# Optimization experiments

Hardware: AMD Instinct MI355X
Metric: run time of the kernel (lower is better)

## Reference

```python
import jax, jax.numpy as jnp
import numpy as np

IN_DIM = 100
OUT_DIM = 200
N_ETYPES = 4
N_STEPS = 8
CONCAT = IN_DIM + OUT_DIM  # 300
EPS = 1e-5


def setup_inputs() -> dict:
    key = jax.random.key(0)
    ks = jax.random.split(key, 24)
    N, E = 100000, 1600000
    rn = lambda k, shape, s=0.05: jax.random.normal(k, shape, dtype=jnp.float32) * s
    return {
        "features": rn(ks[0], (N, IN_DIM), 1.0),
        "edge_index": jax.random.randint(ks[1], (2, E), 0, N, dtype=jnp.int32),
        "edge_types": jax.random.randint(ks[2], (E,), 0, N_ETYPES, dtype=jnp.int32),
        "ggnn_W": rn(ks[3], (N_ETYPES, OUT_DIM, OUT_DIM)),
        "ggnn_b": rn(ks[4], (N_ETYPES, OUT_DIM)),
        "gru_Wih": rn(ks[5], (3 * OUT_DIM, OUT_DIM)),
        "gru_Whh": rn(ks[6], (3 * OUT_DIM, OUT_DIM)),
        "gru_bih": rn(ks[7], (3 * OUT_DIM,)),
        "gru_bhh": rn(ks[8], (3 * OUT_DIM,)),
        "conv1_w": rn(ks[9], (OUT_DIM, OUT_DIM, 3)),
        "conv1_b": rn(ks[10], (OUT_DIM,)),
        "conv2_w": rn(ks[11], (OUT_DIM, OUT_DIM, 1)),
        "conv2_b": rn(ks[12], (OUT_DIM,)),
        "convc1_w": rn(ks[13], (CONCAT, CONCAT, 3)),
        "convc1_b": rn(ks[14], (CONCAT,)),
        "convc2_w": rn(ks[15], (CONCAT, CONCAT, 1)),
        "convc2_b": rn(ks[16], (CONCAT,)),
        "bn_y_g": jnp.ones((OUT_DIM,), jnp.float32),
        "bn_y_b": jnp.zeros((OUT_DIM,), jnp.float32),
        "bn_c_g": jnp.ones((CONCAT,), jnp.float32),
        "bn_c_b": jnp.zeros((CONCAT,), jnp.float32),
        "mlp_y_w": rn(ks[17], (2, OUT_DIM)),
        "mlp_y_b": rn(ks[18], (2,)),
        "mlp_z_w": rn(ks[19], (2, CONCAT)),
        "mlp_z_b": rn(ks[20], (2,)),
    }


def _ggnn(features, src, dst, etypes, W, b, Wih, Whh, bih, bhh):
    """DGL-style GatedGraphConv: per-etype linear, sum-aggregate, GRU update."""
    N = features.shape[0]
    h0 = jnp.concatenate(
        [features, jnp.zeros((N, OUT_DIM - IN_DIM), features.dtype)], axis=-1)

    def step(h, _):
        # transform every node by every etype weight: [n_etypes, N, OUT_DIM]
        t = jnp.einsum('koh,nh->kno', W, h) + b[:, None, :]
        msg = t[etypes, src]                         # [E, OUT_DIM] gather
        a = jax.ops.segment_sum(msg, dst, num_segments=N)  # scatter-add
        # torch GRUCell
        gi = a @ Wih.T + bih
        gh = h @ Whh.T + bhh
        ir, iz, inn = jnp.split(gi, 3, axis=-1)
        hr, hz, hn = jnp.split(gh, 3, axis=-1)
        r = jax.nn.sigmoid(ir + hr)
        z = jax.nn.sigmoid(iz + hz)
        n = jnp.tanh(inn + r * hn)
        return (1.0 - z) * n + z * h, None

    h, _ = jax.lax.scan(step, h0, None, length=N_STEPS)
    return h


def _bn(x, g, b):  # x: [1, C, L], training-mode BatchNorm1d (biased var)
    m = x.mean(axis=(0, 2), keepdims=True)
    v = x.var(axis=(0, 2), keepdims=True)
    return (x - m) * jax.lax.rsqrt(v + EPS) * g[None, :, None] + b[None, :, None]


def _conv1d(x, w, b):  # x: [N, C, L], w: [O, I, k]
    y = jax.lax.conv_general_dilated(
        x, w, window_strides=(1,), padding='VALID',
        dimension_numbers=('NCH', 'OIH', 'NCH'))
    return y + b[None, :, None]


def _maxpool1d(x, k, s):
    return jax.lax.reduce_window(x, -jnp.inf, jax.lax.max,
                                 (1, 1, k), (1, 1, s), 'VALID')


def reference(features, edge_index, edge_types, ggnn_W, ggnn_b,
              gru_Wih, gru_Whh, gru_bih, gru_bhh,
              conv1_w, conv1_b, conv2_w, conv2_b,
              convc1_w, convc1_b, convc2_w, convc2_b,
              bn_y_g, bn_y_b, bn_c_g, bn_c_b,
              mlp_y_w, mlp_y_b, mlp_z_w, mlp_z_b):
    src, dst = edge_index[0], edge_index[1]
    out = _ggnn(features, src, dst, edge_types, ggnn_W, ggnn_b,
                gru_Wih, gru_Whh, gru_bih, gru_bhh)   # [N, 200]
    x_i = features[None]            # [1, N, 100]
    h_i = out[None]                 # [1, N, 200]
    c_i = jnp.concatenate([h_i, x_i], axis=-1)  # [1, N, 300]

    y = _maxpool1d(jax.nn.relu(_bn(_conv1d(jnp.swapaxes(h_i, 1, 2), conv1_w, conv1_b), bn_y_g, bn_y_b)), 3, 2)
    Y2 = jnp.swapaxes(_maxpool1d(jax.nn.relu(_bn(_conv1d(y, conv2_w, conv2_b), bn_y_g, bn_y_b)), 2, 2), 1, 2)

    z = _maxpool1d(jax.nn.relu(_bn(_conv1d(jnp.swapaxes(c_i, 1, 2), convc1_w, convc1_b), bn_c_g, bn_c_b)), 3, 2)
    Z2 = jnp.swapaxes(_maxpool1d(jax.nn.relu(_bn(_conv1d(z, convc2_w, convc2_b), bn_c_g, bn_c_b)), 2, 2), 1, 2)

    before_avg = (Y2 @ mlp_y_w.T + mlp_y_b) * (Z2 @ mlp_z_w.T + mlp_z_b)  # [1, L, 2]
    return jax.nn.sigmoid(before_avg.mean(axis=1))  # [1, 2]
```

## Files before the change

kernel.cpp:

```cpp
#include <hip/hip_runtime.h>
#include <cstddef>
#include <cstdint>


typedef unsigned short u16;
typedef unsigned char u8;
typedef __attribute__((ext_vector_type(8))) short bf16x8;
typedef __attribute__((ext_vector_type(4))) float f32x4;
typedef __attribute__((ext_vector_type(2))) float f32x2;

static __device__ __forceinline__ float bf2f(u16 u) {
  union { unsigned int i; float f; } v; v.i = ((unsigned int)u) << 16; return v.f;
}
static __device__ __forceinline__ u16 f2bf(float f) {
  union { float f; unsigned int i; } v; v.f = f;
  unsigned int r = v.i + 0x7FFFu + ((v.i >> 16) & 1u);
  return (u16)(r >> 16);
}
static __device__ __forceinline__ float sigm(float x) { return 1.f / (1.f + __expf(-x)); }
static __device__ __forceinline__ u8 f2fp8(float x) {
  return (u8)(__builtin_amdgcn_cvt_pk_fp8_f32(x, 0.f, 0, false) & 0xff);
}

static __device__ __forceinline__ void gload16(const void* gp, void* lp) {
  __builtin_amdgcn_global_load_lds(
      (const __attribute__((address_space(1))) void*)gp,
      (__attribute__((address_space(3))) void*)lp, 16, 0, 0);
}

__global__ void fail_k(float* out, float code) { out[0] = code; out[1] = code; }

__global__ void init_hb_k(const float* __restrict__ feat, u16* __restrict__ hb, int N) {
  int total = N * 224;
  for (int i = blockIdx.x * blockDim.x + threadIdx.x; i < total; i += blockDim.x * gridDim.x) {
    int n = i / 224, c = i - n * 224;
    hb[i] = (c < 100) ? f2bf(feat[(size_t)n * 100 + c]) : (u16)0;
  }
}

__global__ void init_hq_k(const float* __restrict__ feat, u8* __restrict__ ahq, int N) {
  int total = N * 224;
  for (int i = blockIdx.x * blockDim.x + threadIdx.x; i < total; i += blockDim.x * gridDim.x) {
    int n = i / 224, c = i - n * 224;
    ahq[(size_t)n * 448 + 224 + c] = (c < 100) ? f2fp8(feat[(size_t)n * 100 + c]) : (u8)0;
  }
}

__global__ void count_deg_k(const int* __restrict__ dst, const int* __restrict__ et,
                            int* __restrict__ deg_et, int N, int E) {
  for (int e = blockIdx.x * blockDim.x + threadIdx.x; e < E; e += blockDim.x * gridDim.x)
    atomicAdd(&deg_et[et[e] * N + dst[e]], 1);
}

__global__ __launch_bounds__(1024) void bsum_k(const int* __restrict__ cnt,
                                               int* __restrict__ bsum, int L) {
  __shared__ int buf[1024];
  int i = blockIdx.x * 1024 + threadIdx.x;
  buf[threadIdx.x] = (i < L) ? cnt[i] : 0;
  __syncthreads();
  for (int o = 512; o > 0; o >>= 1) {
    if (threadIdx.x < o) buf[threadIdx.x] += buf[threadIdx.x + o];
    __syncthreads();
  }
  if (threadIdx.x == 0) bsum[blockIdx.x] = buf[0];
}

__global__ __launch_bounds__(1024) void scanb_k(int* __restrict__ bsum, int nb) {
  __shared__ int buf[1024];
  int v = (threadIdx.x < nb) ? bsum[threadIdx.x] : 0;
  buf[threadIdx.x] = v;
  __syncthreads();
  for (int o = 1; o < 1024; o <<= 1) {
    int t = (threadIdx.x >= o) ? buf[threadIdx.x - o] : 0;
    __syncthreads();
    buf[threadIdx.x] += t;
    __syncthreads();
  }
  if (threadIdx.x < nb) bsum[threadIdx.x] = buf[threadIdx.x] - v;
}

__global__ __launch_bounds__(1024) void scan_fin_k(const int* __restrict__ cnt,
                                                   const int* __restrict__ bsum,
                                                   int* __restrict__ off, int L) {
  __shared__ int buf[1024];
  int i = blockIdx.x * 1024 + threadIdx.x;
  int v = (i < L) ? cnt[i] : 0;
  buf[threadIdx.x] = v;
  __syncthreads();
  for (int o = 1; o < 1024; o <<= 1) {
    int t = (threadIdx.x >= o) ? buf[threadIdx.x - o] : 0;
    __syncthreads();
    buf[threadIdx.x] += t;
    __syncthreads();
  }
  if (i < L) off[i] = buf[threadIdx.x] - v + bsum[blockIdx.x];
}

__global__ void copy_int_k(const int* __restrict__ a, int* __restrict__ b, int n) {
  for (int i = blockIdx.x * blockDim.x + threadIdx.x; i < n; i += blockDim.x * gridDim.x) b[i] = a[i];
}

__global__ void fill_src_k(const int* __restrict__ src, const int* __restrict__ dst,
                           const int* __restrict__ et, int* __restrict__ cursor,
                           int* __restrict__ esrc, int N, int E) {
  for (int e = blockIdx.x * blockDim.x + threadIdx.x; e < E; e += blockDim.x * gridDim.x) {
    int p = atomicAdd(&cursor[et[e] * N + dst[e]], 1);
    esrc[p] = src[e];
  }
}


__global__ void pack_wcat8_k(const float* __restrict__ W, const float* __restrict__ gb,
                             u8* __restrict__ dst) {
  int total = 200 * 832;
  for (int i = blockIdx.x * blockDim.x + threadIdx.x; i < total; i += blockDim.x * gridDim.x) {
    int o = i / 832, kp = i - o * 832;
    float v = 0.f;
    if (kp < 800) { int k = kp / 200, kk = kp - k * 200; v = W[((size_t)k * 200 + o) * 200 + kk]; }
    else if (kp < 804) v = gb[(kp - 800) * 200 + o];
    dst[i] = f2fp8(v);
  }
}

__global__ void pack_wall8_k(const float* __restrict__ Wih, const float* __restrict__ Whh,
                             u8* __restrict__ dst) {
  int total = 800 * 448;
  for (int i = blockIdx.x * blockDim.x + threadIdx.x; i < total; i += blockDim.x * gridDim.x) {
    int jp = i / 448, kp = i - jp * 448;
    int o = jp >> 2, g = jp & 3;
    float v = 0.f;
    if (g == 0) {
      if (kp < 200) v = Wih[(size_t)o * 200 + kp];
      else if (kp >= 224 && kp < 424) v = Whh[(size_t)o * 200 + (kp - 224)];
    } else if (g == 1) {
      if (kp < 200) v = Wih[(size_t)(200 + o) * 200 + kp];
      else if (kp >= 224 && kp < 424) v = Whh[(size_t)(200 + o) * 200 + (kp - 224)];
    } else if (g == 2) {
      if (kp < 200) v = Wih[(size_t)(400 + o) * 200 + kp];
    } else {
      if (kp >= 224 && kp < 424) v = Whh[(size_t)(400 + o) * 200 + (kp - 224)];
    }
    dst[i] = f2fp8(v);
  }
}

__global__ void ball_i_k(const float* __restrict__ bih, const float* __restrict__ bhh,
                         float* __restrict__ ball) {
  int j = blockIdx.x * blockDim.x + threadIdx.x;
  if (j < 800) {
    int o = j >> 2, g = j & 3;
    float v;
    if (g == 0) v = bih[o] + bhh[o];
    else if (g == 1) v = bih[200 + o] + bhh[200 + o];
    else if (g == 2) v = bih[400 + o];
    else v = bhh[400 + o];
    ball[j] = v;
  }
}

__global__ void pack_lin_b(const float* __restrict__ src, u16* __restrict__ dst,
                           int Nn, int K, int Kp) {
  int total = Nn * Kp;
  for (int i = blockIdx.x * blockDim.x + threadIdx.x; i < total; i += blockDim.x * gridDim.x) {
    int o = i / Kp, kp = i - o * Kp;
    dst[i] = (kp < K) ? f2bf(src[(size_t)o * K + kp]) : (u16)0;
  }
}

__global__ void pack_w1c_k(const float* __restrict__ src, u16* __restrict__ dst) {
  int total = 200 * 1056;
  for (int i = blockIdx.x * blockDim.x + threadIdx.x; i < total; i += blockDim.x * gridDim.x) {
    int o = i / 1056, r = i - o * 1056;
    int t = r / 352, kp = r - t * 352;
    dst[i] = (kp < 200) ? f2bf(src[((size_t)o * 200 + kp) * 3 + t]) : (u16)0;
  }
}

__global__ void pack_wc1_b(const float* __restrict__ src, u16* __restrict__ dst) {
  int total = 300 * 1056;
  for (int i = blockIdx.x * blockDim.x + threadIdx.x; i < total; i += blockDim.x * gridDim.x) {
    int o = i / 1056, r = i - o * 1056;
    int t = r / 352, kp = r - t * 352;
    int ci = (kp < 224) ? (kp < 200 ? kp : -1) : ((kp - 224) < 100 ? 200 + (kp - 224) : -1);
    dst[i] = (ci >= 0) ? f2bf(src[((size_t)o * 300 + ci) * 3 + t]) : (u16)0;
  }
}

__global__ void agg8_k(const int* __restrict__ off_et, const int* __restrict__ deg_et,
                       const int* __restrict__ esrc, const u8* __restrict__ ahq,
                       u8* __restrict__ scat8, int N) {
  int gtid = blockIdx.x * blockDim.x + threadIdx.x;
  int wid = gtid >> 6, lane = threadIdx.x & 63;
  int nw = (blockDim.x * gridDim.x) >> 6;
  int sub = lane >> 4, l = lane & 15;
  int total = N * 4;
  for (int u = wid; u < total; u += nw) {
    int n = u >> 2, k = u & 3;
    u8* srow = scat8 + (size_t)n * 832;
    int rs = off_et[(size_t)k * N + n], d = deg_et[(size_t)k * N + n];
    f32x2 a2[8];
#pragma unroll
    for (int j = 0; j < 8; ++j) a2[j] = (f32x2)0.f;
    if (l < 13) {
      for (int i = sub; i < d; i += 4) {
        const u8* hr = ahq + (size_t)esrc[rs + i] * 448 + 224 + l * 16;
        uint4 v = *reinterpret_cast<const uint4*>(hr);
        a2[0] += __builtin_amdgcn_cvt_pk_f32_fp8(v.x, 0);
        a2[1] += __builtin_amdgcn_cvt_pk_f32_fp8(v.x, 1);
        a2[2] += __builtin_amdgcn_cvt_pk_f32_fp8(v.y, 0);
        a2[3] += __builtin_amdgcn_cvt_pk_f32_fp8(v.y, 1);
        a2[4] += __builtin_amdgcn_cvt_pk_f32_fp8(v.z, 0);
        a2[5] += __builtin_amdgcn_cvt_pk_f32_fp8(v.z, 1);
        a2[6] += __builtin_amdgcn_cvt_pk_f32_fp8(v.w, 0);
        a2[7] += __builtin_amdgcn_cvt_pk_f32_fp8(v.w, 1);
      }
    }
#pragma unroll
    for (int j = 0; j < 8; ++j) {
      a2[j][0] += __shfl_xor(a2[j][0], 16);
      a2[j][1] += __shfl_xor(a2[j][1], 16);
      a2[j][0] += __shfl_xor(a2[j][0], 32);
      a2[j][1] += __shfl_xor(a2[j][1], 32);
    }
    if (sub == 0 && l < 13) {
      int d0, d1, d2, d3;
      d0 = __builtin_amdgcn_cvt_pk_fp8_f32(a2[0][0], a2[0][1], 0, false);
      d0 = __builtin_amdgcn_cvt_pk_fp8_f32(a2[1][0], a2[1][1], d0, true);
      d1 = __builtin_amdgcn_cvt_pk_fp8_f32(a2[2][0], a2[2][1], 0, false);
      d1 = __builtin_amdgcn_cvt_pk_fp8_f32(a2[3][0], a2[3][1], d1, true);
      *reinterpret_cast<uint2*>(srow + k * 200 + l * 16) = make_uint2(d0, d1);
      if (l < 12) {
        d2 = __builtin_amdgcn_cvt_pk_fp8_f32(a2[4][0], a2[4][1], 0, false);
        d2 = __builtin_amdgcn_cvt_pk_fp8_f32(a2[5][0], a2[5][1], d2, true);
        d3 = __builtin_amdgcn_cvt_pk_fp8_f32(a2[6][0], a2[6][1], 0, false);
        d3 = __builtin_amdgcn_cvt_pk_fp8_f32(a2[7][0], a2[7][1], d3, true);
        *reinterpret_cast<uint2*>(srow + k * 200 + l * 16 + 8) = make_uint2(d2, d3);
      }
    }
    if (k == 0 && lane == 13) {
      float g0 = (float)deg_et[(size_t)0 * N + n];
      float g1 = (float)deg_et[(size_t)1 * N + n];
      float g2 = (float)deg_et[(size_t)2 * N + n];
      float g3 = (float)deg_et[(size_t)3 * N + n];
      int rr = __builtin_amdgcn_cvt_pk_fp8_f32(g0, g1, 0, false);
      rr = __builtin_amdgcn_cvt_pk_fp8_f32(g2, g3, rr, true);
      *reinterpret_cast<unsigned*>(srow + 800) = (unsigned)rr;
    }
    if (k == 3 && lane >= 32 && lane < 39)
      *reinterpret_cast<unsigned*>(srow + 804 + (lane - 32) * 4) = 0;
  }
}

__global__ __launch_bounds__(512, 4) void gemm_a8(
    const u8* __restrict__ A, int lda,
    const u8* __restrict__ B, int ldb,
    u8* __restrict__ Cq, int ldcb, int npad,
    int M, int Nn, int K, int gyr) {
  const int gx = gridDim.x;
  int lin = blockIdx.y * gx + blockIdx.x;
  int k8 = lin & 7, j = lin >> 3;
  int band = gridDim.y >> 3;
  int yy = j / gx, xx = j - yy * gx;
  int by = k8 * band + yy;
  if (by >= gyr) return;
  const int m0 = by * 256, n0 = xx * 128;

  __shared__ __align__(16) u8 As[3 * 8192];
  __shared__ __align__(16) u8 Bs[3 * 4096];
  const int tid = threadIdx.x;
  const int lane = tid & 63;
  const int w = tid >> 6;
  const int wr = w >> 1, wc = w & 1;
  const int fr = lane & 15;
  const int g = lane >> 4;

  const int rowA = tid >> 1;
  const int cA = (tid & 1) ^ (rowA & 1);
  int gaA = m0 + rowA; if (gaA >= M) gaA = M - 1;
  const u8* pa = A + (size_t)gaA * lda + cA * 16;
  u8* lA = &As[(size_t)(w * 64) * 16];
  const int sB = w * 32 + (lane & 31);
  const int rowB = sB >> 1;
  const int cB = (sB & 1) ^ (rowB & 1);
  int gbB = n0 + rowB; if (gbB >= Nn) gbB = Nn - 1;
  const u8* pb = B + (size_t)gbB * ldb + cB * 16;
  u8* lB = &Bs[(size_t)(w * 32) * 16];
  const bool doB = (lane < 32);

  const int rdoff = (((g >> 1) ^ (fr & 1)) << 4) + ((g & 1) << 3);

  f32x4 acc[4][4] = {};
  const int nt = K >> 5;
  const int ABUF = 8192, BBUF = 4096;

  gload16(pa, lA);
  if (doB) gload16(pb, lB);
  pa += 32; pb += 32;
  if (nt > 1) {
    gload16(pa, lA + ABUF);
    if (doB) gload16(pb, lB + BBUF);
    pa += 32; pb += 32;
  }

  for (int t = 0; t < nt; ++t) {
    if (t + 1 < nt) asm volatile("s_waitcnt vmcnt(2)" ::: "memory");
    else            asm volatile("s_waitcnt vmcnt(0)" ::: "memory");
    __builtin_amdgcn_s_barrier();
    if (t + 2 < nt) {
      int bi = (t + 2) % 3;
      gload16(pa, lA + bi * ABUF);
      if (doB) gload16(pb, lB + bi * BBUF);
      pa += 32; pb += 32;
    }
    int ca = (t % 3) * ABUF, cbb = (t % 3) * BBUF;
    long af[4], bfv[4];
#pragma unroll
    for (int i = 0; i < 4; ++i) {
      int row = wr * 64 + i * 16 + fr;
      af[i] = *reinterpret_cast<const long*>(&As[ca + row * 32 + rdoff]);
    }
#pragma unroll
    for (int jj = 0; jj < 4; ++jj) {
      int row = wc * 64 + jj * 16 + fr;
      bfv[jj] = *reinterpret_cast<const long*>(&Bs[cbb + row * 32 + rdoff]);
    }
    __builtin_amdgcn_s_setprio(1);
#pragma unroll
    for (int i = 0; i < 4; ++i)
#pragma unroll
      for (int jj = 0; jj < 4; ++jj)
        acc[i][jj] = __builtin_amdgcn_mfma_f32_16x16x32_fp8_fp8(af[i], bfv[jj], acc[i][jj], 0, 0, 0);
    __builtin_amdgcn_s_setprio(0);
  }

  const int er = (lane >> 4) * 4;
  const int ec = lane & 15;
#pragma unroll
  for (int i = 0; i < 4; ++i) {
#pragma unroll
    for (int jj = 0; jj < 4; ++jj) {
      int n = n0 + wc * 64 + jj * 16 + ec;
#pragma unroll
      for (int r = 0; r < 4; ++r) {
        int m = m0 + wr * 64 + i * 16 + er + r;
        if (m >= M) continue;
        if (n < Nn) Cq[(size_t)m * ldcb + n] = f2fp8(acc[i][jj][r]);
        else if (n < npad) Cq[(size_t)m * ldcb + n] = (u8)0;
      }
    }
  }
}

__global__ __launch_bounds__(512, 4) void gemm_gru8(
    const u8* __restrict__ A, int lda,
    const u8* __restrict__ B, int ldb,
    int M, int K, const float* __restrict__ bias,
    u16* __restrict__ hb, u8* __restrict__ hq, int gyr) {
  const int gx = gridDim.x;
  int lin = blockIdx.y * gx + blockIdx.x;
  int k8 = lin & 7, j = lin >> 3;
  int band = gridDim.y >> 3;
  int yy = j / gx, xx = j - yy * gx;
  int by = k8 * band + yy;
  if (by >= gyr) return;
  const int m0 = by * 256, n0 = xx * 128;
  const int Nn = 800;

  __shared__ __align__(16) u8 SM8[65536];
  u8* As = SM8;
  u8* Bs = SM8 + 24576;
  const int tid = threadIdx.x;
  const int lane = tid & 63;
  const int w = tid >> 6;
  const int wr = w >> 1, wc = w & 1;
  const int fr = lane & 15;
  const int g = lane >> 4;

  const int rowA = tid >> 1;
  const int cA = (tid & 1) ^ (rowA & 1);
  int gaA = m0 + rowA; if (gaA >= M) gaA = M - 1;
  const u8* pa = A + (size_t)gaA * lda + cA * 16;
  u8* lA = &As[(size_t)(w * 64) * 16];
  const int sB = w * 32 + (lane & 31);
  const int rowB = sB >> 1;
  const int cB = (sB & 1) ^ (rowB & 1);
  int gbB = n0 + rowB; if (gbB >= Nn) gbB = Nn - 1;
  const u8* pb = B + (size_t)gbB * ldb + cB * 16;
  u8* lB = &Bs[(size_t)(w * 32) * 16];
  const bool doB = (lane < 32);

  const int rdoff = (((g >> 1) ^ (fr & 1)) << 4) + ((g & 1) << 3);

  f32x4 acc[4][4] = {};
  const int nt = K >> 5;
  const int ABUF = 8192, BBUF = 4096;

  gload16(pa, lA);
  if (doB) gload16(pb, lB);
  pa += 32; pb += 32;
  if (nt > 1) {
    gload16(pa, lA + ABUF);
    if (doB) gload16(pb, lB + BBUF);
    pa += 32; pb += 32;
  }

  for (int t = 0; t < nt; ++t) {
    if (t + 1 < nt) asm volatile("s_waitcnt vmcnt(2)" ::: "memory");
    else            asm volatile("s_waitcnt vmcnt(0)" ::: "memory");
    __builtin_amdgcn_s_barrier();
    if (t + 2 < nt) {
      int bi = (t + 2) % 3;
      gload16(pa, lA + bi * ABUF);
      if (doB) gload16(pb, lB + bi * BBUF);
      pa += 32; pb += 32;
    }
    int ca = (t % 3) * ABUF, cbb = (t % 3) * BBUF;
    long af[4], bfv[4];
#pragma unroll
    for (int i = 0; i < 4; ++i) {
      int row = wr * 64 + i * 16 + fr;
      af[i] = *reinterpret_cast<const long*>(&As[ca + row * 32 + rdoff]);
    }
#pragma unroll
    for (int jj = 0; jj < 4; ++jj) {
      int row = wc * 64 + jj * 16 + fr;
      bfv[jj] = *reinterpret_cast<const long*>(&Bs[cbb + row * 32 + rdoff]);
    }
    __builtin_amdgcn_s_setprio(1);
#pragma unroll
    for (int i = 0; i < 4; ++i)
#pragma unroll
      for (int jj = 0; jj < 4; ++jj)
        acc[i][jj] = __builtin_amdgcn_mfma_f32_16x16x32_fp8_fp8(af[i], bfv[jj], acc[i][jj], 0, 0, 0);
    __builtin_amdgcn_s_setprio(0);
  }

  const int er = (lane >> 4) * 4;
  const int ec = lane & 15;
  __syncthreads();
  float* ep = (float*)(SM8) + (size_t)w * 2048;

  for (int hh = 0; hh < 2; ++hh) {
#pragma unroll
    for (int jj2 = 0; jj2 < 2; ++jj2) {
      int jj = hh * 2 + jj2;
      int n = n0 + wc * 64 + jj * 16 + ec;
      float bv = (n < 800) ? bias[n] : 0.f;
#pragma unroll
      for (int i = 0; i < 4; ++i)
#pragma unroll
        for (int r = 0; r < 4; ++r) {
          int row_loc = i * 16 + er + r;
          ep[row_loc * 32 + jj2 * 16 + ec] = acc[i][jj][r] + bv;
        }
    }
    __syncthreads();
#pragma unroll
    for (int p = 0; p < 8; ++p) {
      int idx = p * 64 + lane;
      int row = idx >> 3, og = idx & 7;
      int n_base = n0 + wc * 64 + hh * 32 + og * 4;
      int m = m0 + wr * 64 + row;
      if (n_base < 800 && m < M) {
        f32x4 gv = *reinterpret_cast<f32x4*>(&ep[row * 32 + og * 4]);
        float rg = sigm(gv[0]);
        float zg = sigm(gv[1]);
        float x = gv[2] + rg * gv[3];
        float e2 = __expf(2.f * x);
        float nn = (e2 - 1.f) / (e2 + 1.f);
        int o = n_base >> 2;
        float hold = bf2f(hb[(size_t)m * 224 + o]);
        float hv = (1.f - zg) * nn + zg * hold;
        hb[(size_t)m * 224 + o] = f2bf(hv);
        hq[(size_t)m * 224 + o] = f2fp8(hv);
      }
    }
    __syncthreads();
  }
}

__global__ void hcopy8_k(const u8* __restrict__ hq, u8* __restrict__ ahq, int N) {
  int total = N * 50;
  for (int i = blockIdx.x * blockDim.x + threadIdx.x; i < total; i += blockDim.x * gridDim.x) {
    int n = i / 50, o4 = (i - n * 50) * 4;
    *reinterpret_cast<unsigned*>(ahq + (size_t)n * 448 + 224 + o4) =
        *reinterpret_cast<const unsigned*>(hq + (size_t)n * 224 + o4);
  }
}

__global__ __launch_bounds__(512, 4) void gemm_mfma(
    const u16* __restrict__ A, int lda,
    const u16* __restrict__ B, int ldb,
    u16* __restrict__ Cb, int ldcb, int npad,
    int M, int Nn, int K, const float* __restrict__ bias, int gyr) {
  const int gx = gridDim.x;
  int lin = blockIdx.y * gx + blockIdx.x;
  int k8 = lin & 7, j = lin >> 3;
  int band = gridDim.y >> 3;
  int yy = j / gx, xx = j - yy * gx;
  int by = k8 * band + yy;
  if (by >= gyr) return;
  const int m0 = by * 256, n0 = xx * 128;

  __shared__ __align__(16) u16 As[3 * 8192];
  __shared__ __align__(16) u16 Bs[3 * 4096];
  const int tid = threadIdx.x;
  const int lane = tid & 63;
  const int w = tid >> 6;
  const int wr = w >> 1, wc = w & 1;
  const int fr = lane & 15;
  const int g = lane >> 4;

  const int sA0 = w * 64 + lane, sA1 = sA0 + 512, sB = sA0;
  int rA0 = sA0 >> 2, cA0 = (sA0 & 3) ^ ((rA0 >> 1) & 3);
  int rA1 = sA1 >> 2, cA1 = (sA1 & 3) ^ ((rA1 >> 1) & 3);
  int rB  = sB  >> 2, cB  = (sB & 3) ^ ((rB >> 1) & 3);
  int ga0 = m0 + rA0; if (ga0 >= M) ga0 = M - 1;
  int ga1 = m0 + rA1; if (ga1 >= M) ga1 = M - 1;
  int gb  = n0 + rB;  if (gb >= Nn) gb = Nn - 1;
  const u16* pa0 = A + (size_t)ga0 * lda + cA0 * 8;
  const u16* pa1 = A + (size_t)ga1 * lda + cA1 * 8;
  const u16* pb  = B + (size_t)gb  * ldb + cB * 8;
  u16* lA0 = &As[(w * 64) * 8];
  u16* lA1 = &As[(512 + w * 64) * 8];
  u16* lB  = &Bs[(w * 64) * 8];

  const int gxr = g ^ ((fr >> 1) & 3);

  f32x4 acc[4][4] = {};
  const int nt = K >> 5;
  const int ABUF = 8192, BBUF = 4096;

  gload16(pa0, lA0); gload16(pa1, lA1); gload16(pb, lB);
  pa0 += 32; pa1 += 32; pb += 32;
  if (nt > 1) {
    gload16(pa0, lA0 + ABUF); gload16(pa1, lA1 + ABUF); gload16(pb, lB + BBUF);
    pa0 += 32; pa1 += 32; pb += 32;
  }

  for (int t = 0; t < nt; ++t) {
    if (t + 1 < nt) asm volatile("s_waitcnt vmcnt(3)" ::: "memory");
    else            asm volatile("s_waitcnt vmcnt(0)" ::: "memory");
    __builtin_amdgcn_s_barrier();
    if (t + 2 < nt) {
      int bi = (t + 2) % 3;
      gload16(pa0, lA0 + bi * ABUF); gload16(pa1, lA1 + bi * ABUF); gload16(pb, lB + bi * BBUF);
      pa0 += 32; pa1 += 32; pb += 32;
    }
    int ca = (t % 3) * ABUF, cbb = (t % 3) * BBUF;
    bf16x8 af[4], bfv[4];
#pragma unroll
    for (int i = 0; i < 4; ++i) {
      int row = wr * 64 + i * 16 + fr;
      af[i] = *reinterpret_cast<const bf16x8*>(&As[ca + (row * 4 + gxr) * 8]);
    }
#pragma unroll
    for (int jj = 0; jj < 4; ++jj) {
      int row = wc * 64 + jj * 16 + fr;
      bfv[jj] = *reinterpret_cast<const bf16x8*>(&Bs[cbb + (row * 4 + gxr) * 8]);
    }
    __builtin_amdgcn_s_setprio(1);
#pragma unroll
    for (int i = 0; i < 4; ++i)
#pragma unroll
      for (int jj = 0; jj < 4; ++jj)
        acc[i][jj] = __builtin_amdgcn_mfma_f32_16x16x32_bf16(af[i], bfv[jj], acc[i][jj], 0, 0, 0);
    __builtin_amdgcn_s_setprio(0);
  }

  const int er = (lane >> 4) * 4;
  const int ec = lane & 15;
#pragma unroll
  for (int i = 0; i < 4; ++i) {
#pragma unroll
    for (int jj = 0; jj < 4; ++jj) {
      int n = n0 + wc * 64 + jj * 16 + ec;
#pragma unroll
      for (int r = 0; r < 4; ++r) {
        int m = m0 + wr * 64 + i * 16 + er + r;
        if (m >= M) continue;
        if (n < Nn) {
          float v = acc[i][jj][r];
          if (bias) v += bias[n];
          Cb[(size_t)m * ldcb + n] = f2bf(v);
        } else if (n < npad) {
          Cb[(size_t)m * ldcb + n] = (u16)0;
        }
      }
    }
  }
}

__global__ void cmat_k(const u16* __restrict__ hb, const float* __restrict__ feat,
                       u16* __restrict__ c, int N) {
  int total = N * 352;
  for (int i = blockIdx.x * blockDim.x + threadIdx.x; i < total; i += blockDim.x * gridDim.x) {
    int n = i / 352, j = i - n * 352;
    u16 v;
    if (j < 224) v = hb[(size_t)n * 224 + j];
    else { int f = j - 224; v = (f < 100) ? f2bf(feat[(size_t)n * 100 + f]) : (u16)0; }
    c[i] = v;
  }
}

__global__ __launch_bounds__(1024) void bn_stats2_k(const u16* __restrict__ X, int L, int C,
                                                    float* __restrict__ stats) {
  const int Q = 1024 / C;
  const int T = Q * C;
  const int tid = threadIdx.x;
  float s = 0.f, q = 0.f;
  int c = 0;
  if (tid < T) {
    int qi = tid / C; c = tid - qi * C;
    for (size_t r = (size_t)blockIdx.x * Q + qi; r < (size_t)L; r += (size_t)gridDim.x * Q) {
      float v = bf2f(X[r * C + c]);
      s += v; q += v * v;
    }
  }
  __shared__ float sb[304], qb[304];
  for (int cc = tid; cc < C; cc += 1024) { sb[cc] = 0.f; qb[cc] = 0.f; }
  __syncthreads();
  if (tid < T) { atomicAdd(&sb[c], s); atomicAdd(&qb[c], q); }
  __syncthreads();
  for (int cc = tid; cc < C; cc += 1024) {
    atomicAdd(&stats[cc], sb[cc]);
    atomicAdd(&stats[C + cc], qb[cc]);
  }
}

__global__ void bn_fin_k(const float* __restrict__ stats, const float* __restrict__ g,
                         const float* __restrict__ b, int C, float Linv,
                         float* __restrict__ scsh) {
  int c = blockIdx.x * blockDim.x + threadIdx.x;
  if (c < C) {
    float mean = stats[c] * Linv;
    float var = stats[C + c] * Linv - mean * mean;
    float sc = g[c] * rsqrtf(var + 1e-5f);
    scsh[c] = sc;
    scsh[C + c] = b[c] - mean * sc;
  }
}

__global__ void pool_bf_k(const u16* __restrict__ X, int C, const float* __restrict__ scsh,
                          int kw, int stride, u16* __restrict__ Y, int Cpad, int Lout) {
  int total = Lout * Cpad;
  for (int i = blockIdx.x * blockDim.x + threadIdx.x; i < total; i += blockDim.x * gridDim.x) {
    int lp = i / Cpad, c = i - lp * Cpad;
    if (c >= C) { Y[i] = (u16)0; continue; }
    float sc = scsh[c], sh = scsh[C + c];
    int l0 = lp * stride;
    float m = 0.f;
    for (int wq = 0; wq < kw; ++wq)
      m = fmaxf(m, fmaf(bf2f(X[(size_t)(l0 + wq) * C + c]), sc, sh));
    Y[i] = f2bf(m);
  }
}

__global__ void pool_f32_k(const u16* __restrict__ X, int C, const float* __restrict__ scsh,
                           int kw, int stride, float* __restrict__ Y, int Lout) {
  int total = Lout * C;
  for (int i = blockIdx.x * blockDim.x + threadIdx.x; i < total; i += blockDim.x * gridDim.x) {
    int lp = i / C, c = i - lp * C;
    float sc = scsh[c], sh = scsh[C + c];
    int l0 = lp * stride;
    float m = 0.f;
    for (int wq = 0; wq < kw; ++wq)
      m = fmaxf(m, fmaf(bf2f(X[(size_t)(l0 + wq) * C + c]), sc, sh));
    Y[i] = m;
  }
}

__global__ __launch_bounds__(256) void final_dot_k(
    const float* __restrict__ Y2, const float* __restrict__ Z2,
    const float* __restrict__ wy, const float* __restrict__ by,
    const float* __restrict__ wz, const float* __restrict__ bz,
    float* __restrict__ acc, int L) {
  float s0 = 0.f, s1 = 0.f;
  for (int lp = blockIdx.x * blockDim.x + threadIdx.x; lp < L; lp += blockDim.x * gridDim.x) {
    const float* y = Y2 + (size_t)lp * 200;
    const float* z = Z2 + (size_t)lp * 300;
    float d0 = 0.f, d1 = 0.f;
    for (int k = 0; k < 200; ++k) { float v = y[k]; d0 += v * wy[k]; d1 += v * wy[200 + k]; }
    float e0 = 0.f, e1 = 0.f;
    for (int k = 0; k < 300; ++k) { float v = z[k]; e0 += v * wz[k]; e1 += v * wz[300 + k]; }
    s0 += (d0 + by[0]) * (e0 + bz[0]);
    s1 += (d1 + by[1]) * (e1 + bz[1]);
  }
  __shared__ float r0[256], r1[256];
  r0[threadIdx.x] = s0; r1[threadIdx.x] = s1;
  __syncthreads();
  for (int off = 128; off > 0; off >>= 1) {
    if (threadIdx.x < off) { r0[threadIdx.x] += r0[threadIdx.x + off]; r1[threadIdx.x] += r1[threadIdx.x + off]; }
    __syncthreads();
  }
  if (threadIdx.x == 0) { atomicAdd(&acc[0], r0[0]); atomicAdd(&acc[1], r1[0]); }
}

__global__ void final_out_k(const float* __restrict__ acc, float invL, float* __restrict__ out) {
  int j = threadIdx.x;
  if (j < 2) out[j] = 1.f / (1.f + expf(-acc[j] * invL));
}


static inline void gemmL(hipStream_t st, const u16* A, int lda, const u16* B, int ldb,
                         u16* Cb, int ldcb, int npad, int M, int Nn, int K, const float* bias) {
  int ncols = (npad > Nn) ? npad : Nn;
  int gx = (ncols + 127) / 128;
  int gy = (M + 255) / 256;
  int gyp = ((gy + 7) / 8) * 8;
  dim3 g(gx, gyp);
  gemm_mfma<<<g, 512, 0, st>>>(A, lda, B, ldb, Cb, ldcb, npad, M, Nn, K, bias, gy);
}

extern "C" void kernel_launch(void* const* d_in, const int* in_sizes, int n_in,
                              void* d_out, int out_size, void* d_ws, size_t ws_size,
                              hipStream_t stream) {
  (void)n_in; (void)out_size;
  const float* feat    = (const float*)d_in[0];
  const int*   eix     = (const int*)d_in[1];
  const int*   etyp    = (const int*)d_in[2];
  const float* ggnnW   = (const float*)d_in[3];
  const float* ggnnB   = (const float*)d_in[4];
  const float* Wih     = (const float*)d_in[5];
  const float* Whh     = (const float*)d_in[6];
  const float* bih     = (const float*)d_in[7];
  const float* bhh     = (const float*)d_in[8];
  const float* conv1w  = (const float*)d_in[9];
  const float* conv2w  = (const float*)d_in[11];
  const float* convc1w = (const float*)d_in[13];
  const float* convc2w = (const float*)d_in[15];
  const float* bnyg    = (const float*)d_in[17];
  const float* bnyb    = (const float*)d_in[18];
  const float* bncg    = (const float*)d_in[19];
  const float* bncb    = (const float*)d_in[20];
  const float* mlpyw   = (const float*)d_in[21];
  const float* mlpyb   = (const float*)d_in[22];
  const float* mlpzw   = (const float*)d_in[23];
  const float* mlpzb   = (const float*)d_in[24];

  const int N = in_sizes[0] / 100;
  const int E = in_sizes[2];
  const int* src = eix;
  const int* dst = eix + E;

  char* base = (char*)d_ws;
  const size_t AHQ_B = (size_t)N * 448;
  const size_t HB_B  = (size_t)N * 224 * 2;
  const int CH = (N + 1) / 2;
  const size_t SCR_B = (size_t)CH * 1664;

  u8*  ahq = (u8*)base;
  u16* hb  = (u16*)(base + AHQ_B);
  char* R1 = base + AHQ_B + HB_B;
  char* WREG = R1 + SCR_B;

  u8*  Wcat8 = (u8*)WREG;
  u8*  Wall8 = Wcat8 + 166400;
  u16* w1c   = (u16*)(Wall8 + 358400);
  u16* c2b   = w1c + 211200;
  u16* wc1   = c2b + 44800;
  u16* wc2   = wc1 + 316800;
  float* ball  = (float*)(wc2 + 96000);
  float* stats = ball + 832;
  float* scsh  = stats + 600;
  float* acc2  = scsh + 600;
  int* deg_et = (int*)(acc2 + 8);
  int* off_et = deg_et + 4 * (size_t)N;
  int* cursor = off_et + 4 * (size_t)N;
  int* esrc   = cursor + 4 * (size_t)N;
  int* bsum   = esrc + E;
  const int L4 = 4 * N;
  const int NB = (L4 + 1023) / 1024;
  size_t need = (size_t)((char*)(bsum + NB) - base);

  if (ws_size < need) {
    fail_k<<<1, 64, 0, stream>>>((float*)d_out, -(float)(ws_size >> 20));
    return;
  }

  hipMemsetAsync(deg_et, 0, sizeof(int) * 4 * (size_t)N, stream);
  init_hb_k<<<2048, 256, 0, stream>>>(feat, hb, N);
  init_hq_k<<<2048, 256, 0, stream>>>(feat, ahq, N);
  count_deg_k<<<2048, 256, 0, stream>>>(dst, etyp, deg_et, N, E);
  bsum_k<<<NB, 1024, 0, stream>>>(deg_et, bsum, L4);
  scanb_k<<<1, 1024, 0, stream>>>(bsum, NB);
  scan_fin_k<<<NB, 1024, 0, stream>>>(deg_et, bsum, off_et, L4);
  copy_int_k<<<512, 256, 0, stream>>>(off_et, cursor, L4);
  fill_src_k<<<2048, 256, 0, stream>>>(src, dst, etyp, cursor, esrc, N, E);
  pack_wcat8_k<<<651, 256, 0, stream>>>(ggnnW, ggnnB, Wcat8);
  pack_wall8_k<<<1400, 256, 0, stream>>>(Wih, Whh, Wall8);
  ball_i_k<<<4, 256, 0, stream>>>(bih, bhh, ball);
  pack_w1c_k<<<825, 256, 0, stream>>>(conv1w, w1c);
  pack_lin_b<<<175, 256, 0, stream>>>(conv2w, c2b, 200, 200, 224);
  pack_wc1_b<<<1238, 256, 0, stream>>>(convc1w, wc1);
  pack_lin_b<<<375, 256, 0, stream>>>(convc2w, wc2, 300, 300, 320);

  u8* scat8   = (u8*)R1;
  u8* hq_next = (u8*)R1;

  const int gy = (N + 255) / 256;
  const int gyp = ((gy + 7) / 8) * 8;

  for (int step = 0; step < 8; ++step) {
    agg8_k<<<4096, 256, 0, stream>>>(off_et, deg_et, esrc, ahq, scat8, N);
    gemm_a8<<<dim3(2, gyp), 512, 0, stream>>>(scat8, 832, Wcat8, 832,
                                              ahq, 448, 224, N, 200, 832, gy);
    gemm_gru8<<<dim3(7, gyp), 512, 0, stream>>>(ahq, 448, Wall8, 448, N, 448, ball,
                                                hb, hq_next, gy);
    hcopy8_k<<<2048, 256, 0, stream>>>(hq_next, ahq, N);
  }

  const int L1 = N - 2;
  const int L2 = (L1 - 3) / 2 + 1;
  const int L3 = (L2 - 2) / 2 + 1;

  u16* cmat = (u16*)R1;
  u16* out1 = (u16*)base;
  size_t y1_off = (((size_t)L1 * 400) + 255) & ~(size_t)255;
  u16* y1 = (u16*)(base + y1_off);
  size_t o2_off = y1_off + ((((size_t)L2 * 448) + 255) & ~(size_t)255);
  u16* out2 = (u16*)(base + o2_off);
  float* Y2f = (float*)base;
  size_t oc1_off = (((size_t)L3 * 800) + 255) & ~(size_t)255;
  u16* outc1 = (u16*)(base + oc1_off);
  u16* z1 = (u16*)R1;
  size_t oc2_off = (((size_t)L2 * 640) + 255) & ~(size_t)255;
  u16* outc2 = (u16*)(R1 + oc2_off);
  float* Z2f = (float*)(base + oc1_off);

  cmat_k<<<4096, 256, 0, stream>>>(hb, feat, cmat, N);

  gemmL(stream, cmat, 352, w1c, 1056, out1, 200, 200, L1, 200, 1056, nullptr);
  hipMemsetAsync(stats, 0, sizeof(float) * 400, stream);
  bn_stats2_k<<<512, 1024, 0, stream>>>(out1, L1, 200, stats);
  bn_fin_k<<<2, 256, 0, stream>>>(stats, bnyg, bnyb, 200, 1.f / (float)L1, scsh);
  pool_bf_k<<<2048, 256, 0, stream>>>(out1, 200, scsh, 3, 2, y1, 224, L2);

  gemmL(stream, y1, 224, c2b, 224, out2, 200, 200, L2, 200, 224, nullptr);
  hipMemsetAsync(stats, 0, sizeof(float) * 400, stream);
  bn_stats2_k<<<512, 1024, 0, stream>>>(out2, L2, 200, stats);
  bn_fin_k<<<2, 256, 0, stream>>>(stats, bnyg, bnyb, 200, 1.f / (float)L2, scsh);
  pool_f32_k<<<2048, 256, 0, stream>>>(out2, 200, scsh, 2, 2, Y2f, L3);

  gemmL(stream, cmat, 352, wc1, 1056, outc1, 300, 300, L1, 300, 1056, nullptr);
  hipMemsetAsync(stats, 0, sizeof(float) * 600, stream);
  bn_stats2_k<<<512, 1024, 0, stream>>>(outc1, L1, 300, stats);
  bn_fin_k<<<2, 256, 0, stream>>>(stats, bncg, bncb, 300, 1.f / (float)L1, scsh);
  pool_bf_k<<<2048, 256, 0, stream>>>(outc1, 300, scsh, 3, 2, z1, 320, L2);

  gemmL(stream, z1, 320, wc2, 320, outc2, 300, 300, L2, 300, 320, nullptr);
  hipMemsetAsync(stats, 0, sizeof(float) * 600, stream);
  bn_stats2_k<<<512, 1024, 0, stream>>>(outc2, L2, 300, stats);
  bn_fin_k<<<2, 256, 0, stream>>>(stats, bncg, bncb, 300, 1.f / (float)L2, scsh);
  pool_f32_k<<<2048, 256, 0, stream>>>(outc2, 300, scsh, 2, 2, Z2f, L3);

  hipMemsetAsync(acc2, 0, sizeof(float) * 2, stream);
  final_dot_k<<<256, 256, 0, stream>>>(Y2f, Z2f, mlpyw, mlpyb, mlpzw, mlpzb, acc2, L3);
  final_out_k<<<1, 64, 0, stream>>>(acc2, 1.f / (float)L3, (float*)d_out);
}
```

Before: 3.504 ms.

## Gather from dense fp8 hidden buffer and assign one node per wave in aggregation

Keeps a separate dense N×224 fp8 copy of the hidden state, which the GRU GEMM writes directly instead of into scratch. The aggregation kernel gathers neighbor rows from this compact buffer. It now processes one node per wave, with each 16-lane group handling one edge type, which removes the cross-lane shuffle reduction. This avoids the wide strided rows and the reduction overhead, but adds extra workspace and can cause load imbalance across lane groups when per-type degrees differ.

```diff
diff --git a/kernel.cpp b/kernel.cpp
--- a/kernel.cpp
+++ b/kernel.cpp
@@ -38,11 +38,14 @@
   }
 }
 
-__global__ void init_hq_k(const float* __restrict__ feat, u8* __restrict__ ahq, int N) {
+__global__ void init_hq_k(const float* __restrict__ feat, u8* __restrict__ hqd,
+                          u8* __restrict__ ahq, int N) {
   int total = N * 224;
   for (int i = blockIdx.x * blockDim.x + threadIdx.x; i < total; i += blockDim.x * gridDim.x) {
     int n = i / 224, c = i - n * 224;
-    ahq[(size_t)n * 448 + 224 + c] = (c < 100) ? f2fp8(feat[(size_t)n * 100 + c]) : (u8)0;
+    u8 v = (c < 100) ? f2fp8(feat[(size_t)n * 100 + c]) : (u8)0;
+    hqd[i] = v;
+    ahq[(size_t)n * 448 + 224 + c] = v;
   }
 }
 
@@ -187,23 +190,22 @@
 }
 
 __global__ void agg8_k(const int* __restrict__ off_et, const int* __restrict__ deg_et,
-                       const int* __restrict__ esrc, const u8* __restrict__ ahq,
+                       const int* __restrict__ esrc, const u8* __restrict__ hqd,
                        u8* __restrict__ scat8, int N) {
   int gtid = blockIdx.x * blockDim.x + threadIdx.x;
   int wid = gtid >> 6, lane = threadIdx.x & 63;
   int nw = (blockDim.x * gridDim.x) >> 6;
   int sub = lane >> 4, l = lane & 15;
-  int total = N * 4;
-  for (int u = wid; u < total; u += nw) {
-    int n = u >> 2, k = u & 3;
+  for (int n = wid; n < N; n += nw) {
     u8* srow = scat8 + (size_t)n * 832;
-    int rs = off_et[(size_t)k * N + n], d = deg_et[(size_t)k * N + n];
+    int rs = off_et[(size_t)sub * N + n];
+    int d  = deg_et[(size_t)sub * N + n];
     f32x2 a2[8];
 #pragma unroll
     for (int j = 0; j < 8; ++j) a2[j] = (f32x2)0.f;
-    if (l < 13) {
-      for (int i = sub; i < d; i += 4) {
-        const u8* hr = ahq + (size_t)esrc[rs + i] * 448 + 224 + l * 16;
+    for (int i = 0; i < d; ++i) {
+      if (l < 13) {
+        const u8* hr = hqd + (size_t)esrc[rs + i] * 224 + l * 16;
         uint4 v = *reinterpret_cast<const uint4*>(hr);
         a2[0] += __builtin_amdgcn_cvt_pk_f32_fp8(v.x, 0);
         a2[1] += __builtin_amdgcn_cvt_pk_f32_fp8(v.x, 1);
@@ -215,29 +217,23 @@
         a2[7] += __builtin_amdgcn_cvt_pk_f32_fp8(v.w, 1);
       }
     }
-#pragma unroll
-    for (int j = 0; j < 8; ++j) {
-      a2[j][0] += __shfl_xor(a2[j][0], 16);
-      a2[j][1] += __shfl_xor(a2[j][1], 16);
-      a2[j][0] += __shfl_xor(a2[j][0], 32);
-      a2[j][1] += __shfl_xor(a2[j][1], 32);
-    }
-    if (sub == 0 && l < 13) {
-      int d0, d1, d2, d3;
+    if (l < 13) {
+      int d0, d1;
       d0 = __builtin_amdgcn_cvt_pk_fp8_f32(a2[0][0], a2[0][1], 0, false);
       d0 = __builtin_amdgcn_cvt_pk_fp8_f32(a2[1][0], a2[1][1], d0, true);
       d1 = __builtin_amdgcn_cvt_pk_fp8_f32(a2[2][0], a2[2][1], 0, false);
       d1 = __builtin_amdgcn_cvt_pk_fp8_f32(a2[3][0], a2[3][1], d1, true);
-      *reinterpret_cast<uint2*>(srow + k * 200 + l * 16) = make_uint2(d0, d1);
+      *reinterpret_cast<uint2*>(srow + sub * 200 + l * 16) = make_uint2(d0, d1);
       if (l < 12) {
+        int d2, d3;
         d2 = __builtin_amdgcn_cvt_pk_fp8_f32(a2[4][0], a2[4][1], 0, false);
         d2 = __builtin_amdgcn_cvt_pk_fp8_f32(a2[5][0], a2[5][1], d2, true);
         d3 = __builtin_amdgcn_cvt_pk_fp8_f32(a2[6][0], a2[6][1], 0, false);
         d3 = __builtin_amdgcn_cvt_pk_fp8_f32(a2[7][0], a2[7][1], d3, true);
-        *reinterpret_cast<uint2*>(srow + k * 200 + l * 16 + 8) = make_uint2(d2, d3);
+        *reinterpret_cast<uint2*>(srow + sub * 200 + l * 16 + 8) = make_uint2(d2, d3);
       }
     }
-    if (k == 0 && lane == 13) {
+    if (sub == 0 && l == 13) {
       float g0 = (float)deg_et[(size_t)0 * N + n];
       float g1 = (float)deg_et[(size_t)1 * N + n];
       float g2 = (float)deg_et[(size_t)2 * N + n];
@@ -246,8 +242,8 @@
       rr = __builtin_amdgcn_cvt_pk_fp8_f32(g2, g3, rr, true);
       *reinterpret_cast<unsigned*>(srow + 800) = (unsigned)rr;
     }
-    if (k == 3 && lane >= 32 && lane < 39)
-      *reinterpret_cast<unsigned*>(srow + 804 + (lane - 32) * 4) = 0;
+    if (sub == 3 && l >= 1 && l <= 7)
+      *reinterpret_cast<unsigned*>(srow + 804 + (l - 1) * 4) = 0;
   }
 }
 
@@ -746,12 +742,14 @@
   char* base = (char*)d_ws;
   const size_t AHQ_B = (size_t)N * 448;
   const size_t HB_B  = (size_t)N * 224 * 2;
+  const size_t HQD_B = (size_t)N * 224;
   const int CH = (N + 1) / 2;
   const size_t SCR_B = (size_t)CH * 1664;
 
   u8*  ahq = (u8*)base;
   u16* hb  = (u16*)(base + AHQ_B);
-  char* R1 = base + AHQ_B + HB_B;
+  u8*  hqd = (u8*)(base + AHQ_B + HB_B);
+  char* R1 = base + AHQ_B + HB_B + HQD_B;
   char* WREG = R1 + SCR_B;
 
   u8*  Wcat8 = (u8*)WREG;
@@ -780,7 +778,7 @@
 
   hipMemsetAsync(deg_et, 0, sizeof(int) * 4 * (size_t)N, stream);
   init_hb_k<<<2048, 256, 0, stream>>>(feat, hb, N);
-  init_hq_k<<<2048, 256, 0, stream>>>(feat, ahq, N);
+  init_hq_k<<<2048, 256, 0, stream>>>(feat, hqd, ahq, N);
   count_deg_k<<<2048, 256, 0, stream>>>(dst, etyp, deg_et, N, E);
   bsum_k<<<NB, 1024, 0, stream>>>(deg_et, bsum, L4);
   scanb_k<<<1, 1024, 0, stream>>>(bsum, NB);
@@ -795,19 +793,18 @@
   pack_wc1_b<<<1238, 256, 0, stream>>>(convc1w, wc1);
   pack_lin_b<<<375, 256, 0, stream>>>(convc2w, wc2, 300, 300, 320);
 
-  u8* scat8   = (u8*)R1;
-  u8* hq_next = (u8*)R1;
+  u8* scat8 = (u8*)R1;
 
   const int gy = (N + 255) / 256;
   const int gyp = ((gy + 7) / 8) * 8;
 
   for (int step = 0; step < 8; ++step) {
-    agg8_k<<<4096, 256, 0, stream>>>(off_et, deg_et, esrc, ahq, scat8, N);
+    agg8_k<<<4096, 256, 0, stream>>>(off_et, deg_et, esrc, hqd, scat8, N);
     gemm_a8<<<dim3(2, gyp), 512, 0, stream>>>(scat8, 832, Wcat8, 832,
                                               ahq, 448, 224, N, 200, 832, gy);
     gemm_gru8<<<dim3(7, gyp), 512, 0, stream>>>(ahq, 448, Wall8, 448, N, 448, ball,
-                                                hb, hq_next, gy);
-    hcopy8_k<<<2048, 256, 0, stream>>>(hq_next, ahq, N);
+                                                hb, hqd, gy);
+    hcopy8_k<<<2048, 256, 0, stream>>>(hqd, ahq, N);
   }
 
   const int L1 = N - 2;
```

New measurement: 3.043 ms. 1.15x faster.
